# Optimization experiments

Measured on AMD Instinct MI355X. Metric: run time of the kernel, lower is better.

The kernel has to match this reference:

```python
import jax, jax.numpy as jnp
import numpy as np

SIZE = 48
DIST = 6
PAD = DIST // 2
DESIZE = SIZE - 4  # 44
CONVEY = 0.9
RATE = 5
BATCH = 4
FLAT = DESIZE * SIZE * SIZE  # 101376


def setup_inputs() -> dict:
    key = jax.random.key(0)
    ks = jax.random.split(key, 6)
    D, H, W = DESIZE, SIZE, SIZE
    return {
        "vinput": jax.random.normal(ks[0], (BATCH, D, H, W), jnp.float32),
        "frame": jax.random.normal(ks[1], (D, H, W), jnp.float32) * 0.1,
        # 0.05 scale keeps the 216-term recurrent sums ~unit magnitude over RATE steps
        "synapse": jax.random.normal(ks[2], (D, H, W, DIST, DIST, DIST), jnp.float32) * 0.05,
        "W1": jax.random.normal(ks[3], (FLAT, 1024), jnp.float32) * 0.01,
        "b1": jnp.zeros((1024,), jnp.float32),
        "W2": jax.random.normal(ks[4], (1024, 128), jnp.float32) * 0.05,
        "b2": jnp.zeros((128,), jnp.float32),
        "W3": jax.random.normal(ks[5], (128, 10), jnp.float32) * 0.1,
        "b3": jnp.zeros((10,), jnp.float32),
    }


def _local_step(neu, syn_flat, d, p):
    """Locally-connected (unshared-weight) 3D window reduce.
    neu: (B, D, H, W); syn_flat: (D, H, W, d^3).
    For each voxel, weighted sum over its d x d x d padded neighborhood."""
    B, D, H, W = neu.shape
    pad = jnp.pad(neu, ((0, 0), (p, p), (p, p), (p, p)))
    # patches: (B, d^3, D', H', W') with valid windows; keep the first D/H/W starts
    patches = jax.lax.conv_general_dilated_patches(
        pad[:, None], filter_shape=(d, d, d), window_strides=(1, 1, 1), padding="VALID"
    )
    patches = patches[:, :, :D, :H, :W]
    return jnp.einsum("bcijk,ijkc->bijk", patches, syn_flat)


def reference(vinput, frame, synapse, W1, b1, W2, b2, W3, b3):
    D, H, W = frame.shape
    d = synapse.shape[-1]
    p = d // 2
    syn_flat = synapse.reshape(D, H, W, d * d * d)
    neu = vinput + frame  # frame broadcast over batch
    for _ in range(RATE):
        out = _local_step(neu, syn_flat, d, p)
        neu = jax.nn.relu(out) * CONVEY
    x = neu.reshape(neu.shape[0], -1)
    x = jax.nn.relu(x @ W1 + b1)
    x = jax.nn.relu(x @ W2 + b2)
    return x @ W3 + b3
```

## Files before the change

### kernel.cpp

```cpp
#include <hip/hip_runtime.h>

#define SIZE   48
#define DESIZE 44
#define PAD    3
#define BATCH  4
#define FLAT   (DESIZE*SIZE*SIZE)
#define CVOL   216

#define TJ 4
#define TK 16
#define NA 6
#define NB (TJ+5)
#define NC (TK+5)
#define NEU_T (NA*NB*NC)
#define NTILE 1584

#define KSLICE  132
#define NSLICES (FLAT/KSLICE)

template <int CBASE, int CNT>
__device__ __forceinline__ void do_chunk4(const float4* __restrict__ rp,
                                          const float4* __restrict__ neu4,
                                          int lanebase, float acc[4]) {
    constexpr int H1n = (CNT + 1) / 2;
    constexpr int H2n = CNT - H1n;
    {
        float4 sr[H1n];
#pragma unroll
        for (int s2 = 0; s2 < H1n; ++s2) sr[s2] = rp[CBASE + s2];
#pragma unroll
        for (int s2 = 0; s2 < H1n; ++s2) {
#pragma unroll
            for (int j = 0; j < 4; ++j) {
                const int c   = (CBASE + s2) * 4 + j;
                const int off = (c / 36) * (NB * NC) + ((c % 36) / 6) * NC + (c % 6);
                const float wv = (&sr[s2].x)[j];
                const float4 n4 = neu4[lanebase + off];
                acc[0] += wv * n4.x; acc[1] += wv * n4.y;
                acc[2] += wv * n4.z; acc[3] += wv * n4.w;
            }
        }
    }
    {
        float4 sr[H2n];
#pragma unroll
        for (int s2 = 0; s2 < H2n; ++s2) sr[s2] = rp[CBASE + H1n + s2];
#pragma unroll
        for (int s2 = 0; s2 < H2n; ++s2) {
#pragma unroll
            for (int j = 0; j < 4; ++j) {
                const int c   = (CBASE + H1n + s2) * 4 + j;
                const int off = (c / 36) * (NB * NC) + ((c % 36) / 6) * NC + (c % 6);
                const float wv = (&sr[s2].x)[j];
                const float4 n4 = neu4[lanebase + off];
                acc[0] += wv * n4.x; acc[1] += wv * n4.y;
                acc[2] += wv * n4.z; acc[3] += wv * n4.w;
            }
        }
    }
}

template <bool FIRST>
__global__ __launch_bounds__(256, 4) void k_step(const float4* __restrict__ nin4,
                                                 const float* __restrict__ vin,
                                                 const float* __restrict__ frame,
                                                 const float* __restrict__ syn,
                                                 float4* __restrict__ nout4) {
    __shared__ float4 neu4[NEU_T];
    __shared__ float  part[4 * 256];
    int t  = threadIdx.x;
    int r  = blockIdx.x;
    int i0 = r / 36;
    int r2 = r % 36;
    int j0 = (r2 / 3) * TJ;
    int k0 = (r2 % 3) * TK;

    for (int e = t; e < NEU_T; e += 256) {
        int a   = e / (NB * NC);
        int rem = e % (NB * NC);
        int jj  = rem / NC;
        int cc  = rem % NC;
        int gi = i0 + a - PAD;
        int gj = j0 + jj - PAD;
        int gk = k0 + cc - PAD;
        float4 vv = make_float4(0.f, 0.f, 0.f, 0.f);
        if ((unsigned)gi < DESIZE && (unsigned)gj < SIZE && (unsigned)gk < SIZE) {
            int idx = (gi * SIZE + gj) * SIZE + gk;
            if (FIRST) {
                float fr = frame[idx];
                vv.x = vin[0 * FLAT + idx] + fr;
                vv.y = vin[1 * FLAT + idx] + fr;
                vv.z = vin[2 * FLAT + idx] + fr;
                vv.w = vin[3 * FLAT + idx] + fr;
            } else {
                vv = nin4[idx];
            }
        }
        neu4[e] = vv;
    }
    __syncthreads();

    int w = t >> 6, l = t & 63;
    int dj = l >> 4, dk = l & 15;
    int lanebase = dj * NC + dk;
    const float4* rp = (const float4*)(syn +
        (size_t)((i0 * SIZE + j0 + dj) * SIZE + k0 + dk) * CVOL);

    float acc[4] = {0.f, 0.f, 0.f, 0.f};
    switch (w) {
        case 0:  do_chunk4< 0, 14>(rp, neu4, lanebase, acc); break;
        case 1:  do_chunk4<14, 14>(rp, neu4, lanebase, acc); break;
        case 2:  do_chunk4<28, 13>(rp, neu4, lanebase, acc); break;
        default: do_chunk4<41, 13>(rp, neu4, lanebase, acc); break;
    }
#pragma unroll
    for (int bb = 0; bb < 4; ++bb) part[bb * 256 + t] = acc[bb];
    __syncthreads();

    if (t < 64) {
        float4 o;
        o.x = part[  0 + t] + part[  0 + 64 + t] + part[  0 + 128 + t] + part[  0 + 192 + t];
        o.y = part[256 + t] + part[256 + 64 + t] + part[256 + 128 + t] + part[256 + 192 + t];
        o.z = part[512 + t] + part[512 + 64 + t] + part[512 + 128 + t] + part[512 + 192 + t];
        o.w = part[768 + t] + part[768 + 64 + t] + part[768 + 128 + t] + part[768 + 192 + t];
        o.x = fmaxf(o.x, 0.f) * 0.9f;
        o.y = fmaxf(o.y, 0.f) * 0.9f;
        o.z = fmaxf(o.z, 0.f) * 0.9f;
        o.w = fmaxf(o.w, 0.f) * 0.9f;
        int dj2 = t >> 4, dk2 = t & 15;
        nout4[(i0 * SIZE + (j0 + dj2)) * SIZE + (k0 + dk2)] = o;
    }
}

__global__ __launch_bounds__(256) void k_mlp1(const float4* __restrict__ x4,
                                              const float* __restrict__ W1,
                                              float* __restrict__ partial) {
    __shared__ float xs[KSLICE * 4];
    int t = threadIdx.x;
    int s = blockIdx.x;
    int k0 = s * KSLICE;
    for (int e = t; e < KSLICE; e += 256)
        ((float4*)xs)[e] = x4[k0 + e];
    __syncthreads();
    float acc[4][4] = {};
    const float4* wp = (const float4*)(W1 + (size_t)k0 * 1024) + t;
#pragma unroll 6
    for (int kk = 0; kk < KSLICE; ++kk) {
        float4 w  = wp[(size_t)kk * 256];
        float4 xv = *(const float4*)(xs + kk * 4);
        acc[0][0] += xv.x * w.x; acc[0][1] += xv.x * w.y; acc[0][2] += xv.x * w.z; acc[0][3] += xv.x * w.w;
        acc[1][0] += xv.y * w.x; acc[1][1] += xv.y * w.y; acc[1][2] += xv.y * w.z; acc[1][3] += xv.y * w.w;
        acc[2][0] += xv.z * w.x; acc[2][1] += xv.z * w.y; acc[2][2] += xv.z * w.z; acc[2][3] += xv.z * w.w;
        acc[3][0] += xv.w * w.x; acc[3][1] += xv.w * w.y; acc[3][2] += xv.w * w.z; acc[3][3] += xv.w * w.w;
    }
#pragma unroll
    for (int b = 0; b < 4; ++b) {
        float4 o = make_float4(acc[b][0], acc[b][1], acc[b][2], acc[b][3]);
        *(float4*)(partial + (size_t)s * 4096 + b * 1024 + t * 4) = o;
    }
}

__global__ __launch_bounds__(256) void k_reduce1(const float* __restrict__ partial,
                                                 const float* __restrict__ b1,
                                                 float* __restrict__ h1) {
    __shared__ float red[16][17];
    int t = threadIdx.x;
    int e0 = blockIdx.x * 16;
    int eo = t & 15, sl = t >> 4;
    float acc = 0.f;
    for (int it = 0; it < NSLICES / 16; ++it) {
        int s = sl + 16 * it;
        acc += partial[(size_t)s * 4096 + e0 + eo];
    }
    red[sl][eo] = acc;
    __syncthreads();
    if (t < 16) {
        float a = 0.f;
#pragma unroll
        for (int rr = 0; rr < 16; ++rr) a += red[rr][t];
        int e = e0 + t;
        h1[e] = fmaxf(a + b1[e & 1023], 0.f);
    }
}

__global__ __launch_bounds__(64) void k_mlp2(const float* __restrict__ h1,
                                             const float* __restrict__ W2,
                                             float* __restrict__ partial2) {
    __shared__ float xs[32 * 4];
    int t = threadIdx.x;
    int bid = blockIdx.x;
    int s = bid >> 1, ch = bid & 1;
    int k0 = s * 32;
    for (int e = t; e < 128; e += 64) {
        int kk = e >> 2, b = e & 3;
        xs[e] = h1[b * 1024 + k0 + kk];
    }
    __syncthreads();
    float acc[4] = {0.f, 0.f, 0.f, 0.f};
    int n2 = ch * 64 + t;
#pragma unroll
    for (int kk = 0; kk < 32; ++kk) {
        float w = W2[(size_t)(k0 + kk) * 128 + n2];
        float4 xv = *(const float4*)(xs + kk * 4);
        acc[0] += xv.x * w; acc[1] += xv.y * w; acc[2] += xv.z * w; acc[3] += xv.w * w;
    }
#pragma unroll
    for (int b = 0; b < 4; ++b) partial2[s * 512 + b * 128 + n2] = acc[b];
}

__global__ __launch_bounds__(128) void k_mlp3(const float* __restrict__ partial2,
                                              const float* __restrict__ b2,
                                              const float* __restrict__ W3,
                                              const float* __restrict__ b3,
                                              float* __restrict__ out) {
    __shared__ float h2[512];
    int t = threadIdx.x;
    for (int e = t; e < 512; e += 128) {
        int n2 = e & 127;
        float a = b2[n2];
#pragma unroll 8
        for (int s = 0; s < 32; ++s) a += partial2[s * 512 + e];
        h2[e] = fmaxf(a, 0.f);
    }
    __syncthreads();
    if (t < 40) {
        int b = t / 10, o = t % 10;
        float a = b3[o];
        for (int k = 0; k < 128; ++k) a += h2[b * 128 + k] * W3[k * 10 + o];
        out[b * 10 + o] = a;
    }
}

extern "C" void kernel_launch(void* const* d_in, const int* in_sizes, int n_in,
                              void* d_out, int out_size, void* d_ws, size_t ws_size,
                              hipStream_t stream) {
    const float* vin   = (const float*)d_in[0];
    const float* frame = (const float*)d_in[1];
    const float* syn   = (const float*)d_in[2];
    const float* W1    = (const float*)d_in[3];
    const float* b1    = (const float*)d_in[4];
    const float* W2    = (const float*)d_in[5];
    const float* b2    = (const float*)d_in[6];
    const float* W3    = (const float*)d_in[7];
    const float* b3    = (const float*)d_in[8];
    float* out = (float*)d_out;

    float* ws = (float*)d_ws;
    float* A   = ws;
    float* B   = A + (size_t)BATCH * FLAT;
    float* P1  = B + (size_t)BATCH * FLAT;
    float* H1  = P1 + (size_t)NSLICES * 4096;
    float* P2  = H1 + 4096;

    k_step<true ><<<NTILE, 256, 0, stream>>>(nullptr, vin, frame, syn, (float4*)A);
    k_step<false><<<NTILE, 256, 0, stream>>>((const float4*)A, nullptr, nullptr, syn, (float4*)B);
    k_step<false><<<NTILE, 256, 0, stream>>>((const float4*)B, nullptr, nullptr, syn, (float4*)A);
    k_step<false><<<NTILE, 256, 0, stream>>>((const float4*)A, nullptr, nullptr, syn, (float4*)B);
    k_step<false><<<NTILE, 256, 0, stream>>>((const float4*)B, nullptr, nullptr, syn, (float4*)A);

    k_mlp1<<<NSLICES, 256, 0, stream>>>((const float4*)A, W1, P1);
    k_reduce1<<<256, 256, 0, stream>>>(P1, b1, H1);
    k_mlp2<<<64, 64, 0, stream>>>(H1, W2, P2);
    k_mlp3<<<1, 128, 0, stream>>>(P2, b2, W3, b3, out);
}
```

Before: 702.0 us.

## Prefetch synapse weights before tile load; fuse layer-1 reduce into layer-2 GEMV

In the local-step kernel, each thread now issues global loads for the first seven float4s of its synapse chunk before the shared-memory neighborhood fill. The goal is to overlap weight-load latency with the tile fill and the barrier, at the cost of holding extra registers through the load phase. Separately, the k_reduce1 and k_mlp2 kernels are merged into one 32-block kernel: it reduces the layer-1 partials, applies bias and ReLU in shared memory, then does the layer-2 partial products. This removes a launch and the H1 round-trip, but reduces parallelism in the reduction (each of 128 threads per block sums all 768 slices).

```diff
diff --git a/kernel.cpp b/kernel.cpp
--- a/kernel.cpp
+++ b/kernel.cpp
@@ -19,43 +19,36 @@
 #define NSLICES (FLAT/KSLICE)
 
 template <int CBASE, int CNT>
-__device__ __forceinline__ void do_chunk4(const float4* __restrict__ rp,
+__device__ __forceinline__ void do_chunk4(const float4 pre[7],
+                                          const float4* __restrict__ rp,
                                           const float4* __restrict__ neu4,
                                           int lanebase, float acc[4]) {
-    constexpr int H1n = (CNT + 1) / 2;
-    constexpr int H2n = CNT - H1n;
-    {
-        float4 sr[H1n];
-#pragma unroll
-        for (int s2 = 0; s2 < H1n; ++s2) sr[s2] = rp[CBASE + s2];
-#pragma unroll
-        for (int s2 = 0; s2 < H1n; ++s2) {
-#pragma unroll
-            for (int j = 0; j < 4; ++j) {
-                const int c   = (CBASE + s2) * 4 + j;
-                const int off = (c / 36) * (NB * NC) + ((c % 36) / 6) * NC + (c % 6);
-                const float wv = (&sr[s2].x)[j];
-                const float4 n4 = neu4[lanebase + off];
-                acc[0] += wv * n4.x; acc[1] += wv * n4.y;
-                acc[2] += wv * n4.z; acc[3] += wv * n4.w;
-            }
+    constexpr int H2n = CNT - 7;
+#pragma unroll
+    for (int s2 = 0; s2 < 7; ++s2) {
+#pragma unroll
+        for (int j = 0; j < 4; ++j) {
+            const int c   = (CBASE + s2) * 4 + j;
+            const int off = (c / 36) * (NB * NC) + ((c % 36) / 6) * NC + (c % 6);
+            const float wv = (&pre[s2].x)[j];
+            const float4 n4 = neu4[lanebase + off];
+            acc[0] += wv * n4.x; acc[1] += wv * n4.y;
+            acc[2] += wv * n4.z; acc[3] += wv * n4.w;
         }
     }
-    {
-        float4 sr[H2n];
-#pragma unroll
-        for (int s2 = 0; s2 < H2n; ++s2) sr[s2] = rp[CBASE + H1n + s2];
-#pragma unroll
-        for (int s2 = 0; s2 < H2n; ++s2) {
-#pragma unroll
-            for (int j = 0; j < 4; ++j) {
-                const int c   = (CBASE + H1n + s2) * 4 + j;
-                const int off = (c / 36) * (NB * NC) + ((c % 36) / 6) * NC + (c % 6);
-                const float wv = (&sr[s2].x)[j];
-                const float4 n4 = neu4[lanebase + off];
-                acc[0] += wv * n4.x; acc[1] += wv * n4.y;
-                acc[2] += wv * n4.z; acc[3] += wv * n4.w;
-            }
+    float4 sr[H2n];
+#pragma unroll
+    for (int s2 = 0; s2 < H2n; ++s2) sr[s2] = rp[CBASE + 7 + s2];
+#pragma unroll
+    for (int s2 = 0; s2 < H2n; ++s2) {
+#pragma unroll
+        for (int j = 0; j < 4; ++j) {
+            const int c   = (CBASE + 7 + s2) * 4 + j;
+            const int off = (c / 36) * (NB * NC) + ((c % 36) / 6) * NC + (c % 6);
+            const float wv = (&sr[s2].x)[j];
+            const float4 n4 = neu4[lanebase + off];
+            acc[0] += wv * n4.x; acc[1] += wv * n4.y;
+            acc[2] += wv * n4.z; acc[3] += wv * n4.w;
         }
     }
 }
@@ -74,6 +67,16 @@
     int r2 = r % 36;
     int j0 = (r2 / 3) * TJ;
     int k0 = (r2 % 3) * TK;
+
+    int w = t >> 6, l = t & 63;
+    int dj = l >> 4, dk = l & 15;
+    int lanebase = dj * NC + dk;
+    const float4* rp = (const float4*)(syn +
+        (size_t)((i0 * SIZE + j0 + dj) * SIZE + k0 + dk) * CVOL);
+    const int CB = (w == 0) ? 0 : (w == 1) ? 14 : (w == 2) ? 28 : 41;
+    float4 pre[7];
+#pragma unroll
+    for (int s2 = 0; s2 < 7; ++s2) pre[s2] = rp[CB + s2];
 
     for (int e = t; e < NEU_T; e += 256) {
         int a   = e / (NB * NC);
@@ -100,18 +103,12 @@
     }
     __syncthreads();
 
-    int w = t >> 6, l = t & 63;
-    int dj = l >> 4, dk = l & 15;
-    int lanebase = dj * NC + dk;
-    const float4* rp = (const float4*)(syn +
-        (size_t)((i0 * SIZE + j0 + dj) * SIZE + k0 + dk) * CVOL);
-
     float acc[4] = {0.f, 0.f, 0.f, 0.f};
     switch (w) {
-        case 0:  do_chunk4< 0, 14>(rp, neu4, lanebase, acc); break;
-        case 1:  do_chunk4<14, 14>(rp, neu4, lanebase, acc); break;
-        case 2:  do_chunk4<28, 13>(rp, neu4, lanebase, acc); break;
-        default: do_chunk4<41, 13>(rp, neu4, lanebase, acc); break;
+        case 0:  do_chunk4< 0, 14>(pre, rp, neu4, lanebase, acc); break;
+        case 1:  do_chunk4<14, 14>(pre, rp, neu4, lanebase, acc); break;
+        case 2:  do_chunk4<28, 13>(pre, rp, neu4, lanebase, acc); break;
+        default: do_chunk4<41, 13>(pre, rp, neu4, lanebase, acc); break;
     }
 #pragma unroll
     for (int bb = 0; bb < 4; ++bb) part[bb * 256 + t] = acc[bb];
@@ -160,52 +157,33 @@
     }
 }
 
-__global__ __launch_bounds__(256) void k_reduce1(const float* __restrict__ partial,
-                                                 const float* __restrict__ b1,
-                                                 float* __restrict__ h1) {
-    __shared__ float red[16][17];
-    int t = threadIdx.x;
-    int e0 = blockIdx.x * 16;
-    int eo = t & 15, sl = t >> 4;
-    float acc = 0.f;
-    for (int it = 0; it < NSLICES / 16; ++it) {
-        int s = sl + 16 * it;
-        acc += partial[(size_t)s * 4096 + e0 + eo];
-    }
-    red[sl][eo] = acc;
-    __syncthreads();
-    if (t < 16) {
+__global__ __launch_bounds__(128) void k_red2(const float* __restrict__ partial,
+                                              const float* __restrict__ b1,
+                                              const float* __restrict__ W2,
+                                              float* __restrict__ partial2) {
+    __shared__ float h1s[32 * 4];
+    int t  = threadIdx.x;
+    int s  = blockIdx.x;
+    int k0 = s * 32;
+    {
+        int kk = t & 31, b = t >> 5;
         float a = 0.f;
-#pragma unroll
-        for (int rr = 0; rr < 16; ++rr) a += red[rr][t];
-        int e = e0 + t;
-        h1[e] = fmaxf(a + b1[e & 1023], 0.f);
-    }
-}
-
-__global__ __launch_bounds__(64) void k_mlp2(const float* __restrict__ h1,
-                                             const float* __restrict__ W2,
-                                             float* __restrict__ partial2) {
-    __shared__ float xs[32 * 4];
-    int t = threadIdx.x;
-    int bid = blockIdx.x;
-    int s = bid >> 1, ch = bid & 1;
-    int k0 = s * 32;
-    for (int e = t; e < 128; e += 64) {
-        int kk = e >> 2, b = e & 3;
-        xs[e] = h1[b * 1024 + k0 + kk];
+#pragma unroll 16
+        for (int sl = 0; sl < NSLICES; ++sl)
+            a += partial[(size_t)sl * 4096 + b * 1024 + k0 + kk];
+        h1s[kk * 4 + b] = fmaxf(a + b1[k0 + kk], 0.f);
     }
     __syncthreads();
     float acc[4] = {0.f, 0.f, 0.f, 0.f};
-    int n2 = ch * 64 + t;
-#pragma unroll
-    for (int kk = 0; kk < 32; ++kk) {
-        float w = W2[(size_t)(k0 + kk) * 128 + n2];
-        float4 xv = *(const float4*)(xs + kk * 4);
-        acc[0] += xv.x * w; acc[1] += xv.y * w; acc[2] += xv.z * w; acc[3] += xv.w * w;
-    }
-#pragma unroll
-    for (int b = 0; b < 4; ++b) partial2[s * 512 + b * 128 + n2] = acc[b];
+#pragma unroll
+    for (int k2 = 0; k2 < 32; ++k2) {
+        float wv  = W2[(size_t)(k0 + k2) * 128 + t];
+        float4 xv = *(const float4*)(h1s + k2 * 4);
+        acc[0] += xv.x * wv; acc[1] += xv.y * wv;
+        acc[2] += xv.z * wv; acc[3] += xv.w * wv;
+    }
+#pragma unroll
+    for (int bb = 0; bb < 4; ++bb) partial2[s * 512 + bb * 128 + t] = acc[bb];
 }
 
 __global__ __launch_bounds__(128) void k_mlp3(const float* __restrict__ partial2,
@@ -249,8 +227,7 @@
     float* A   = ws;
     float* B   = A + (size_t)BATCH * FLAT;
     float* P1  = B + (size_t)BATCH * FLAT;
-    float* H1  = P1 + (size_t)NSLICES * 4096;
-    float* P2  = H1 + 4096;
+    float* P2  = P1 + (size_t)NSLICES * 4096;
 
     k_step<true ><<<NTILE, 256, 0, stream>>>(nullptr, vin, frame, syn, (float4*)A);
     k_step<false><<<NTILE, 256, 0, stream>>>((const float4*)A, nullptr, nullptr, syn, (float4*)B);
@@ -259,7 +236,6 @@
     k_step<false><<<NTILE, 256, 0, stream>>>((const float4*)B, nullptr, nullptr, syn, (float4*)A);
 
     k_mlp1<<<NSLICES, 256, 0, stream>>>((const float4*)A, W1, P1);
-    k_reduce1<<<256, 256, 0, stream>>>(P1, b1, H1);
-    k_mlp2<<<64, 64, 0, stream>>>(H1, W2, P2);
+    k_red2<<<32, 128, 0, stream>>>(P1, b1, W2, P2);
     k_mlp3<<<1, 128, 0, stream>>>(P2, b2, W3, b3, out);
 }
```

Result: slower. 1.124 ms (+60.1%).
